# Kernel tuning notes

Hardware: AMD Instinct MI355X
Metric: run time of the kernel (lower is better)

Reference implementation:

```python
import jax, jax.numpy as jnp
import numpy as np

N = 100000
IN_C = 256
OUT_C = 256
E = 500000


def gcn_conv(x, W, b, edges):
    """PyG GCNConv: add self-loops, symmetric D^-1/2 (A+I) D^-1/2 normalization,
    then scatter-add of transformed source features into targets, plus bias."""
    n = x.shape[0]
    loop = jnp.arange(n, dtype=edges.dtype)
    row = jnp.concatenate([edges[0], loop])  # source
    col = jnp.concatenate([edges[1], loop])  # target
    deg = jax.ops.segment_sum(jnp.ones_like(col, dtype=x.dtype), col, num_segments=n)
    dis = jax.lax.rsqrt(deg)  # deg >= 1 after self-loops
    norm = dis[row] * dis[col]  # [E+n]
    h = x @ W  # [n, out]
    msg = h[row] * norm[:, None]  # gather + scale
    return jax.ops.segment_sum(msg, col, num_segments=n) + b


def setup_inputs() -> dict:
    key = jax.random.key(0)
    ks = jax.random.split(key, 24)
    x = jax.random.normal(ks[0], (N, IN_C), dtype=jnp.float32)
    edges00 = jax.random.randint(ks[1], (2, E), 0, N, dtype=jnp.int32)
    edges01 = jax.random.randint(ks[2], (2, E), 0, N, dtype=jnp.int32)
    edges10 = jax.random.randint(ks[3], (2, E), 0, N, dtype=jnp.int32)
    edges11 = jax.random.randint(ks[4], (2, E), 0, N, dtype=jnp.int32)
    t0 = (jax.random.uniform(ks[5], (N,)) > 0.5).astype(jnp.float32)
    t1 = 1.0 - t0
    scale = 1.0 / np.sqrt(IN_C)
    W1 = jax.random.normal(ks[6], (IN_C, OUT_C), dtype=jnp.float32) * scale
    W2 = jax.random.normal(ks[7], (IN_C, OUT_C), dtype=jnp.float32) * scale
    W3 = jax.random.normal(ks[8], (IN_C, OUT_C), dtype=jnp.float32) * scale
    W4 = jax.random.normal(ks[9], (IN_C, OUT_C), dtype=jnp.float32) * scale
    b1 = jnp.zeros((OUT_C,), jnp.float32)
    b2 = jnp.zeros((OUT_C,), jnp.float32)
    b3 = jnp.zeros((OUT_C,), jnp.float32)
    b4 = jnp.zeros((OUT_C,), jnp.float32)
    p0 = jax.random.normal(ks[10], (OUT_C,), dtype=jnp.float32)
    p1 = jax.random.normal(ks[11], (OUT_C,), dtype=jnp.float32)
    p2 = jax.random.normal(ks[12], (OUT_C,), dtype=jnp.float32)
    p3 = jax.random.normal(ks[13], (OUT_C,), dtype=jnp.float32)
    p4 = jax.random.normal(ks[14], (OUT_C,), dtype=jnp.float32)
    p5 = jax.random.normal(ks[15], (OUT_C,), dtype=jnp.float32)
    return dict(x=x, edges00=edges00, edges01=edges01, edges10=edges10, edges11=edges11,
                type0_idx=t0, type1_idx=t1,
                W1=W1, b1=b1, W2=W2, b2=b2, W3=W3, b3=b3, W4=W4, b4=b4,
                p0=p0, p1=p1, p2=p2, p3=p3, p4=p4, p5=p5)


def reference(x, edges00, edges01, edges10, edges11, type0_idx, type1_idx,
              W1, b1, W2, b2, W3, b3, W4, b4, p0, p1, p2, p3, p4, p5):
    # x0/x1: first feature column masked by node type, broadcast over out channels
    x0c = type0_idx * x[:, 0]  # [N]
    x1c = type1_idx * x[:, 0]
    x00 = gcn_conv(x, W1, b1, edges00)
    x01 = gcn_conv(x, W2, b2, edges01)
    x10 = gcn_conv(x, W3, b3, edges10)
    x11 = gcn_conv(x, W4, b4, edges11)
    out = (x0c[:, None] * p0 + x1c[:, None] * p1
           + x00 * p2 + x01 * p3 + x10 * p4 + x11 * p5)
    return out
```

## Files before the change

kernel.cpp:

```cpp
#include <hip/hip_runtime.h>


typedef __bf16 v8bf __attribute__((ext_vector_type(8)));
typedef float v4f __attribute__((ext_vector_type(4)));

__device__ __forceinline__ unsigned short f2bf(float f) {
  unsigned u = __float_as_uint(f);
  u += 0x7fffu + ((u >> 16) & 1u);
  return (unsigned short)(u >> 16);
}
__device__ __forceinline__ float bf2f(unsigned short s) {
  return __uint_as_float(((unsigned)s) << 16);
}
__device__ __forceinline__ void async_ld16(const void* g, void* l) {
  __builtin_amdgcn_global_load_lds((__attribute__((address_space(1))) void*)g,
                                   (__attribute__((address_space(3))) void*)l,
                                   16, 0, 0);
}

__global__ void lc_zero(int* __restrict__ p, int n) {
  int i = blockIdx.x * 256 + threadIdx.x;
  if (i < n) p[i] = 0;
}

__global__ void lc_hist(const int* __restrict__ e0, const int* __restrict__ e1,
                        const int* __restrict__ e2, const int* __restrict__ e3,
                        int* __restrict__ hist, int N, int E) {
  int e = blockIdx.x * 256 + threadIdx.x;
  if (e >= E) return;
  int k = blockIdx.y;
  const int* ed = (k == 0) ? e0 : (k == 1) ? e1 : (k == 2) ? e2 : e3;
  int col = ed[E + e];
  atomicAdd(&hist[k * N + col], 1);
}

__global__ void lc_dis(const int* __restrict__ hist, float* __restrict__ dis, int M) {
  int i = blockIdx.x * 256 + threadIdx.x;
  if (i < M) dis[i] = rsqrtf((float)(hist[i] + 1));
}

__global__ void lc_scan1(const int* __restrict__ in, int* __restrict__ outp,
                         int* __restrict__ bsum, int M) {
  __shared__ int tmp[256];
  int t = threadIdx.x, i = blockIdx.x * 256 + t;
  int v = (i < M) ? in[i] : 0;
  tmp[t] = v;
  __syncthreads();
  for (int off = 1; off < 256; off <<= 1) {
    int add = (t >= off) ? tmp[t - off] : 0;
    __syncthreads();
    tmp[t] += add;
    __syncthreads();
  }
  if (i < M) outp[i] = tmp[t] - v;
  if (t == 255) bsum[blockIdx.x] = tmp[255];
}

__global__ void lc_scan2(int* __restrict__ bsum, int nb) {
  __shared__ int tmp[256];
  __shared__ int carry_s;
  int t = threadIdx.x;
  if (t == 0) carry_s = 0;
  __syncthreads();
  for (int base = 0; base < nb; base += 256) {
    int i = base + t;
    int v = (i < nb) ? bsum[i] : 0;
    tmp[t] = v;
    __syncthreads();
    for (int off = 1; off < 256; off <<= 1) {
      int add = (t >= off) ? tmp[t - off] : 0;
      __syncthreads();
      tmp[t] += add;
      __syncthreads();
    }
    int carry = carry_s;
    int total = tmp[255];
    if (i < nb) bsum[i] = carry + tmp[t] - v;
    __syncthreads();
    if (t == 0) carry_s = carry + total;
    __syncthreads();
  }
}

__global__ void lc_scan3(int* __restrict__ rp, int* __restrict__ cursor,
                         const int* __restrict__ bsum, int M) {
  int i = blockIdx.x * 256 + threadIdx.x;
  if (i < M) {
    int v = rp[i] + bsum[blockIdx.x];
    rp[i] = v;
    cursor[i] = v;
  }
}

__global__ void lc_fill(const int* __restrict__ e0, const int* __restrict__ e1,
                        const int* __restrict__ e2, const int* __restrict__ e3,
                        int* __restrict__ cursor, const float* __restrict__ dis,
                        int2* __restrict__ payload, int N, int E) {
  int e = blockIdx.x * 256 + threadIdx.x;
  if (e >= E) return;
  int k = blockIdx.y;
  const int* ed = (k == 0) ? e0 : (k == 1) ? e1 : (k == 2) ? e2 : e3;
  int src = ed[e], col = ed[E + e];
  int pos = atomicAdd(&cursor[k * N + col], 1);
  float nrm = dis[k * N + src] * dis[k * N + col];
  payload[pos] = make_int2(src, __float_as_int(nrm));
}

__global__ void lc_bias(const float* __restrict__ b1, const float* __restrict__ b2,
                        const float* __restrict__ b3, const float* __restrict__ b4,
                        const float* __restrict__ p2, const float* __restrict__ p3,
                        const float* __restrict__ p4, const float* __restrict__ p5,
                        float* __restrict__ biasc) {
  int c = threadIdx.x;
  biasc[c] = b1[c] * p2[c] + b2[c] * p3[c] + b3[c] * p4[c] + b4[c] * p5[c];
}

__global__ void lc_prep(const float* __restrict__ W1, const float* __restrict__ W2,
                        const float* __restrict__ W3, const float* __restrict__ W4,
                        const float* __restrict__ p2, const float* __restrict__ p3,
                        const float* __restrict__ p4, const float* __restrict__ p5,
                        unsigned short* __restrict__ Wt) {
  int b = blockIdx.x;
  int k = b >> 8, co = b & 255;
  int kk = threadIdx.x;
  const float* W = (k == 0) ? W1 : (k == 1) ? W2 : (k == 2) ? W3 : W4;
  const float* p = (k == 0) ? p2 : (k == 1) ? p3 : (k == 2) ? p4 : p5;
  Wt[(size_t)co * 1024 + k * 256 + kk] = f2bf(W[kk * 256 + co] * p[co]);
}

__global__ void lc_cvt(const float4* __restrict__ x4, ushort4* __restrict__ xb4,
                       const float* __restrict__ t0, const float* __restrict__ t1,
                       float* __restrict__ m0, float* __restrict__ m1, int n4) {
  int i = blockIdx.x * 256 + threadIdx.x;
  if (i >= n4) return;
  float4 v = x4[i];
  ushort4 r;
  r.x = f2bf(v.x); r.y = f2bf(v.y); r.z = f2bf(v.z); r.w = f2bf(v.w);
  xb4[i] = r;
  if ((i & 63) == 0) {
    int n = i >> 6;
    float xc = v.x;
    m0[n] = t0[n] * xc;
    m1[n] = t1[n] * xc;
  }
}

__global__ __launch_bounds__(256) void lc_aggx(
    const unsigned short* __restrict__ xb, unsigned short* __restrict__ Agg,
    int aggw, int kcount, int kbase, const int* __restrict__ rp,
    const int* __restrict__ hist, const float* __restrict__ dis,
    const int2* __restrict__ payload, int N) {
  int t = threadIdx.x;
  int w = t >> 6, lane = t & 63;
  int n, k, koff;
  if (kcount == 4) { n = blockIdx.x; k = w; koff = k * 256; }
  else { n = blockIdx.x * 4 + w; k = kbase; koff = 0; }
  if (n >= N) return;
  int c = lane * 4;
  int idx = k * N + n;

  float dn = dis[idx];
  float s = dn * dn;
  ushort4 hv = *(const ushort4*)&xb[(size_t)n * 256 + c];
  float a0 = bf2f(hv.x) * s, a1 = bf2f(hv.y) * s;
  float a2 = bf2f(hv.z) * s, a3 = bf2f(hv.w) * s;

  int start = rp[idx];
  int cnt = hist[idx];
  int i = 0;
  for (; i + 4 <= cnt; i += 4) {
    int2 e0 = payload[start + i];
    int2 e1 = payload[start + i + 1];
    int2 e2 = payload[start + i + 2];
    int2 e3 = payload[start + i + 3];
    ushort4 g0 = *(const ushort4*)&xb[(size_t)e0.x * 256 + c];
    ushort4 g1 = *(const ushort4*)&xb[(size_t)e1.x * 256 + c];
    ushort4 g2 = *(const ushort4*)&xb[(size_t)e2.x * 256 + c];
    ushort4 g3 = *(const ushort4*)&xb[(size_t)e3.x * 256 + c];
    float n0 = __int_as_float(e0.y), n1 = __int_as_float(e1.y);
    float n2 = __int_as_float(e2.y), n3 = __int_as_float(e3.y);
    a0 += bf2f(g0.x) * n0 + bf2f(g1.x) * n1 + bf2f(g2.x) * n2 + bf2f(g3.x) * n3;
    a1 += bf2f(g0.y) * n0 + bf2f(g1.y) * n1 + bf2f(g2.y) * n2 + bf2f(g3.y) * n3;
    a2 += bf2f(g0.z) * n0 + bf2f(g1.z) * n1 + bf2f(g2.z) * n2 + bf2f(g3.z) * n3;
    a3 += bf2f(g0.w) * n0 + bf2f(g1.w) * n1 + bf2f(g2.w) * n2 + bf2f(g3.w) * n3;
  }
  for (; i < cnt; i++) {
    int2 e0 = payload[start + i];
    ushort4 g0 = *(const ushort4*)&xb[(size_t)e0.x * 256 + c];
    float n0 = __int_as_float(e0.y);
    a0 += bf2f(g0.x) * n0;
    a1 += bf2f(g0.y) * n0;
    a2 += bf2f(g0.z) * n0;
    a3 += bf2f(g0.w) * n0;
  }
  ushort4 r;
  r.x = f2bf(a0); r.y = f2bf(a1); r.z = f2bf(a2); r.w = f2bf(a3);
  *(ushort4*)&Agg[(size_t)n * aggw + koff + c] = r;
}

__global__ __launch_bounds__(256) void lc_gemm(
    const unsigned short* __restrict__ A, int strideA,
    const unsigned short* __restrict__ B, int strideB, int K,
    float* __restrict__ out, int Mrows, int addprev, int doepi,
    const float* __restrict__ m0, const float* __restrict__ m1,
    const float* __restrict__ p0, const float* __restrict__ p1,
    const float* __restrict__ biasc) {
  __shared__ alignas(16) unsigned short As[128 * 32];
  __shared__ alignas(16) unsigned short Bs[128 * 32];
  int t = threadIdx.x;
  int w = t >> 6, lane = t & 63;
  int wm = w & 1, wn = w >> 1;
  int quad = lane >> 4, l16 = lane & 15;
  int row0 = blockIdx.x * 128, col0 = blockIdx.y * 128;

  v4f acc[4][4];
#pragma unroll
  for (int mt = 0; mt < 4; mt++)
#pragma unroll
    for (int nt = 0; nt < 4; nt++) {
      v4f z = {0.f, 0.f, 0.f, 0.f};
      acc[mt][nt] = z;
    }

  for (int kk = 0; kk < K; kk += 32) {
#pragma unroll
    for (int p = 0; p < 2; p++) {
      int cbase = p * 256 + w * 64;
      int cA = cbase + lane;
      int rl = cA >> 2, c16 = cA & 3;
      int grow = row0 + rl;
      if (grow >= Mrows) grow = Mrows - 1;
      async_ld16(A + (size_t)grow * strideA + kk + c16 * 8, &As[cbase * 8]);
      async_ld16(B + (size_t)(col0 + rl) * strideB + kk + c16 * 8, &Bs[cbase * 8]);
    }
    __syncthreads();

    v8bf af[4], bfr[4];
#pragma unroll
    for (int mt = 0; mt < 4; mt++) {
      int r = wm * 64 + mt * 16 + l16;
      af[mt] = *(const v8bf*)&As[r * 32 + quad * 8];
    }
#pragma unroll
    for (int nt = 0; nt < 4; nt++) {
      int n = wn * 64 + nt * 16 + l16;
      bfr[nt] = *(const v8bf*)&Bs[n * 32 + quad * 8];
    }
#pragma unroll
    for (int mt = 0; mt < 4; mt++)
#pragma unroll
      for (int nt = 0; nt < 4; nt++)
        acc[mt][nt] =
            __builtin_amdgcn_mfma_f32_16x16x32_bf16(af[mt], bfr[nt], acc[mt][nt], 0, 0, 0);
    __syncthreads();
  }

  float pc0[4], pc1[4], bc[4];
#pragma unroll
  for (int nt = 0; nt < 4; nt++) {
    int gcol = col0 + wn * 64 + nt * 16 + l16;
    pc0[nt] = doepi ? p0[gcol] : 0.f;
    pc1[nt] = doepi ? p1[gcol] : 0.f;
    bc[nt] = doepi ? biasc[gcol] : 0.f;
  }
#pragma unroll
  for (int mt = 0; mt < 4; mt++)
#pragma unroll
    for (int r = 0; r < 4; r++) {
      int grow = row0 + wm * 64 + mt * 16 + quad * 4 + r;
      if (grow >= Mrows) continue;
      float m0v = 0.f, m1v = 0.f;
      if (doepi) { m0v = m0[grow]; m1v = m1[grow]; }
#pragma unroll
      for (int nt = 0; nt < 4; nt++) {
        int gcol = col0 + wn * 64 + nt * 16 + l16;
        size_t o = (size_t)grow * 256 + gcol;
        float v = acc[mt][nt][r];
        if (addprev) v += out[o];
        if (doepi) v += m0v * pc0[nt] + m1v * pc1[nt] + bc[nt];
        out[o] = v;
      }
    }
}

extern "C" void kernel_launch(void* const* d_in, const int* in_sizes, int n_in,
                              void* d_out, int out_size, void* d_ws, size_t ws_size,
                              hipStream_t stream) {
  const float* x = (const float*)d_in[0];
  const int* e00 = (const int*)d_in[1];
  const int* e01 = (const int*)d_in[2];
  const int* e10 = (const int*)d_in[3];
  const int* e11 = (const int*)d_in[4];
  const float* t0 = (const float*)d_in[5];
  const float* t1 = (const float*)d_in[6];
  const float* W1 = (const float*)d_in[7];
  const float* b1 = (const float*)d_in[8];
  const float* W2 = (const float*)d_in[9];
  const float* b2 = (const float*)d_in[10];
  const float* W3 = (const float*)d_in[11];
  const float* b3 = (const float*)d_in[12];
  const float* W4 = (const float*)d_in[13];
  const float* b4 = (const float*)d_in[14];
  const float* p0 = (const float*)d_in[15];
  const float* p1 = (const float*)d_in[16];
  const float* p2 = (const float*)d_in[17];
  const float* p3 = (const float*)d_in[18];
  const float* p4 = (const float*)d_in[19];
  const float* p5 = (const float*)d_in[20];
  float* out = (float*)d_out;

  int N = in_sizes[0] / 256;
  int E = in_sizes[1] / 2;
  int M4 = 4 * N;
  int nb = (M4 + 255) / 256;

  char* wp = (char*)d_ws;
  auto carve = [&](size_t bytes) {
    void* r = (void*)wp;
    wp += (bytes + 255) & ~(size_t)255;
    return r;
  };
  unsigned short* xb = (unsigned short*)carve((size_t)N * 256 * 2);
  unsigned short* Wt = (unsigned short*)carve((size_t)256 * 1024 * 2);
  int* hist = (int*)carve((size_t)M4 * 4);
  float* dis = (float*)carve((size_t)M4 * 4);
  int* rp = (int*)carve((size_t)M4 * 4);
  int* cursor = (int*)carve((size_t)M4 * 4);
  int* bsum = (int*)carve((size_t)nb * 4);
  float* biasc = (float*)carve(256 * 4);
  float* m0 = (float*)carve((size_t)N * 4);
  float* m1 = (float*)carve((size_t)N * 4);
  int2* payload = (int2*)carve((size_t)4 * E * 8);
  size_t used = (size_t)(wp - (char*)d_ws);
  size_t remain = (ws_size > used) ? ws_size - used : 0;
  bool fat = remain >= (size_t)N * 1024 * 2;
  unsigned short* Agg = (unsigned short*)wp;

  int gE = (E + 255) / 256;
  int gM = (M4 + 255) / 256;

  lc_zero<<<gM, 256, 0, stream>>>(hist, M4);
  lc_hist<<<dim3(gE, 4), 256, 0, stream>>>(e00, e01, e10, e11, hist, N, E);
  lc_dis<<<gM, 256, 0, stream>>>(hist, dis, M4);
  lc_scan1<<<nb, 256, 0, stream>>>(hist, rp, bsum, M4);
  lc_scan2<<<1, 256, 0, stream>>>(bsum, nb);
  lc_scan3<<<nb, 256, 0, stream>>>(rp, cursor, bsum, M4);
  lc_fill<<<dim3(gE, 4), 256, 0, stream>>>(e00, e01, e10, e11, cursor, dis, payload, N, E);
  lc_bias<<<1, 256, 0, stream>>>(b1, b2, b3, b4, p2, p3, p4, p5, biasc);
  lc_prep<<<1024, 256, 0, stream>>>(W1, W2, W3, W4, p2, p3, p4, p5, Wt);
  lc_cvt<<<(N * 64 + 255) / 256, 256, 0, stream>>>((const float4*)x, (ushort4*)xb,
                                                   t0, t1, m0, m1, N * 64);

  int gemm_mb = (N + 127) / 128;
  if (fat) {
    lc_aggx<<<N, 256, 0, stream>>>(xb, Agg, 1024, 4, 0, rp, hist, dis, payload, N);
    lc_gemm<<<dim3(gemm_mb, 2), 256, 0, stream>>>(Agg, 1024, Wt, 1024, 1024, out, N,
                                                  0, 1, m0, m1, p0, p1, biasc);
  } else {
    for (int k = 0; k < 4; k++) {
      lc_aggx<<<(N + 3) / 4, 256, 0, stream>>>(xb, Agg, 256, 1, k, rp, hist, dis,
                                               payload, N);
      lc_gemm<<<dim3(gemm_mb, 2), 256, 0, stream>>>(Agg, 256, Wt + k * 256, 1024, 256,
                                                    out, N, (k > 0) ? 1 : 0,
                                                    (k == 3) ? 1 : 0, m0, m1, p0, p1,
                                                    biasc);
    }
  }
}
```

Before: 720.6 us.

## Fuse aggregation with GEMM and replace CSR scan with fixed-capacity bucket scatter

Replaces the histogram/scan/fill CSR build with a single scatter kernel that writes source indices into fixed-capacity per-node buckets, spilling extras to an overflow list. Aggregation and the MFMA GEMM are fused into one kernel: each wave aggregates 16 node rows per relation into LDS and multiplies them by Wt read directly from global memory, then applies the epilogue. This removes the intermediate Agg buffer round trip and several launches. In exchange, norms are recomputed per edge, B operands are not shared through LDS, overflow handling is a linear scan, and bucket memory scales with CAP.

```diff
diff --git a/kernel.cpp b/kernel.cpp
--- a/kernel.cpp
+++ b/kernel.cpp
@@ -12,98 +12,31 @@
 __device__ __forceinline__ float bf2f(unsigned short s) {
   return __uint_as_float(((unsigned)s) << 16);
 }
-__device__ __forceinline__ void async_ld16(const void* g, void* l) {
-  __builtin_amdgcn_global_load_lds((__attribute__((address_space(1))) void*)g,
-                                   (__attribute__((address_space(3))) void*)l,
-                                   16, 0, 0);
-}
-
-__global__ void lc_zero(int* __restrict__ p, int n) {
-  int i = blockIdx.x * 256 + threadIdx.x;
-  if (i < n) p[i] = 0;
-}
-
-__global__ void lc_hist(const int* __restrict__ e0, const int* __restrict__ e1,
-                        const int* __restrict__ e2, const int* __restrict__ e3,
-                        int* __restrict__ hist, int N, int E) {
+
+__global__ void lc_scatter(const int* __restrict__ e0, const int* __restrict__ e1,
+                           const int* __restrict__ e2, const int* __restrict__ e3,
+                           int* __restrict__ hist, int* __restrict__ payload,
+                           int CAP, int* __restrict__ ovf_cnt, int2* __restrict__ ovf,
+                           int N, int E) {
   int e = blockIdx.x * 256 + threadIdx.x;
   if (e >= E) return;
   int k = blockIdx.y;
   const int* ed = (k == 0) ? e0 : (k == 1) ? e1 : (k == 2) ? e2 : e3;
+  int src = ed[e];
   int col = ed[E + e];
-  atomicAdd(&hist[k * N + col], 1);
+  int idx = k * N + col;
+  int rank = atomicAdd(&hist[idx], 1);
+  if (rank < CAP) {
+    payload[(size_t)idx * CAP + rank] = src;
+  } else {
+    int o = atomicAdd(ovf_cnt, 1);
+    ovf[o] = make_int2(idx, src);
+  }
 }
 
 __global__ void lc_dis(const int* __restrict__ hist, float* __restrict__ dis, int M) {
   int i = blockIdx.x * 256 + threadIdx.x;
   if (i < M) dis[i] = rsqrtf((float)(hist[i] + 1));
-}
-
-__global__ void lc_scan1(const int* __restrict__ in, int* __restrict__ outp,
-                         int* __restrict__ bsum, int M) {
-  __shared__ int tmp[256];
-  int t = threadIdx.x, i = blockIdx.x * 256 + t;
-  int v = (i < M) ? in[i] : 0;
-  tmp[t] = v;
-  __syncthreads();
-  for (int off = 1; off < 256; off <<= 1) {
-    int add = (t >= off) ? tmp[t - off] : 0;
-    __syncthreads();
-    tmp[t] += add;
-    __syncthreads();
-  }
-  if (i < M) outp[i] = tmp[t] - v;
-  if (t == 255) bsum[blockIdx.x] = tmp[255];
-}
-
-__global__ void lc_scan2(int* __restrict__ bsum, int nb) {
-  __shared__ int tmp[256];
-  __shared__ int carry_s;
-  int t = threadIdx.x;
-  if (t == 0) carry_s = 0;
-  __syncthreads();
-  for (int base = 0; base < nb; base += 256) {
-    int i = base + t;
-    int v = (i < nb) ? bsum[i] : 0;
-    tmp[t] = v;
-    __syncthreads();
-    for (int off = 1; off < 256; off <<= 1) {
-      int add = (t >= off) ? tmp[t - off] : 0;
-      __syncthreads();
-      tmp[t] += add;
-      __syncthreads();
-    }
-    int carry = carry_s;
-    int total = tmp[255];
-    if (i < nb) bsum[i] = carry + tmp[t] - v;
-    __syncthreads();
-    if (t == 0) carry_s = carry + total;
-    __syncthreads();
-  }
-}
-
-__global__ void lc_scan3(int* __restrict__ rp, int* __restrict__ cursor,
-                         const int* __restrict__ bsum, int M) {
-  int i = blockIdx.x * 256 + threadIdx.x;
-  if (i < M) {
-    int v = rp[i] + bsum[blockIdx.x];
-    rp[i] = v;
-    cursor[i] = v;
-  }
-}
-
-__global__ void lc_fill(const int* __restrict__ e0, const int* __restrict__ e1,
-                        const int* __restrict__ e2, const int* __restrict__ e3,
-                        int* __restrict__ cursor, const float* __restrict__ dis,
-                        int2* __restrict__ payload, int N, int E) {
-  int e = blockIdx.x * 256 + threadIdx.x;
-  if (e >= E) return;
-  int k = blockIdx.y;
-  const int* ed = (k == 0) ? e0 : (k == 1) ? e1 : (k == 2) ? e2 : e3;
-  int src = ed[e], col = ed[E + e];
-  int pos = atomicAdd(&cursor[k * N + col], 1);
-  float nrm = dis[k * N + src] * dis[k * N + col];
-  payload[pos] = make_int2(src, __float_as_int(nrm));
 }
 
 __global__ void lc_bias(const float* __restrict__ b1, const float* __restrict__ b2,
@@ -145,142 +78,120 @@
   }
 }
 
-__global__ __launch_bounds__(256) void lc_aggx(
-    const unsigned short* __restrict__ xb, unsigned short* __restrict__ Agg,
-    int aggw, int kcount, int kbase, const int* __restrict__ rp,
-    const int* __restrict__ hist, const float* __restrict__ dis,
-    const int2* __restrict__ payload, int N) {
+#define LROW 264
+__global__ __launch_bounds__(256, 2) void lc_fused(
+    const unsigned short* __restrict__ xb, const unsigned short* __restrict__ Wt,
+    const int* __restrict__ payload, int CAP, const int* __restrict__ hist,
+    const float* __restrict__ dis, const int* __restrict__ ovf_cnt,
+    const int2* __restrict__ ovf, const float* __restrict__ m0,
+    const float* __restrict__ m1, const float* __restrict__ p0,
+    const float* __restrict__ p1, const float* __restrict__ biasc,
+    float* __restrict__ out, int N) {
+  __shared__ alignas(16) unsigned short lds[4 * 16 * LROW];
   int t = threadIdx.x;
   int w = t >> 6, lane = t & 63;
-  int n, k, koff;
-  if (kcount == 4) { n = blockIdx.x; k = w; koff = k * 256; }
-  else { n = blockIdx.x * 4 + w; k = kbase; koff = 0; }
-  if (n >= N) return;
+  int quad = lane >> 4, l16 = lane & 15;
+  int row0 = blockIdx.x * 64 + w * 16;
+  unsigned short* A = &lds[w * 16 * LROW];
   int c = lane * 4;
-  int idx = k * N + n;
-
-  float dn = dis[idx];
-  float s = dn * dn;
-  ushort4 hv = *(const ushort4*)&xb[(size_t)n * 256 + c];
-  float a0 = bf2f(hv.x) * s, a1 = bf2f(hv.y) * s;
-  float a2 = bf2f(hv.z) * s, a3 = bf2f(hv.w) * s;
-
-  int start = rp[idx];
-  int cnt = hist[idx];
-  int i = 0;
-  for (; i + 4 <= cnt; i += 4) {
-    int2 e0 = payload[start + i];
-    int2 e1 = payload[start + i + 1];
-    int2 e2 = payload[start + i + 2];
-    int2 e3 = payload[start + i + 3];
-    ushort4 g0 = *(const ushort4*)&xb[(size_t)e0.x * 256 + c];
-    ushort4 g1 = *(const ushort4*)&xb[(size_t)e1.x * 256 + c];
-    ushort4 g2 = *(const ushort4*)&xb[(size_t)e2.x * 256 + c];
-    ushort4 g3 = *(const ushort4*)&xb[(size_t)e3.x * 256 + c];
-    float n0 = __int_as_float(e0.y), n1 = __int_as_float(e1.y);
-    float n2 = __int_as_float(e2.y), n3 = __int_as_float(e3.y);
-    a0 += bf2f(g0.x) * n0 + bf2f(g1.x) * n1 + bf2f(g2.x) * n2 + bf2f(g3.x) * n3;
-    a1 += bf2f(g0.y) * n0 + bf2f(g1.y) * n1 + bf2f(g2.y) * n2 + bf2f(g3.y) * n3;
-    a2 += bf2f(g0.z) * n0 + bf2f(g1.z) * n1 + bf2f(g2.z) * n2 + bf2f(g3.z) * n3;
-    a3 += bf2f(g0.w) * n0 + bf2f(g1.w) * n1 + bf2f(g2.w) * n2 + bf2f(g3.w) * n3;
-  }
-  for (; i < cnt; i++) {
-    int2 e0 = payload[start + i];
-    ushort4 g0 = *(const ushort4*)&xb[(size_t)e0.x * 256 + c];
-    float n0 = __int_as_float(e0.y);
-    a0 += bf2f(g0.x) * n0;
-    a1 += bf2f(g0.y) * n0;
-    a2 += bf2f(g0.z) * n0;
-    a3 += bf2f(g0.w) * n0;
-  }
-  ushort4 r;
-  r.x = f2bf(a0); r.y = f2bf(a1); r.z = f2bf(a2); r.w = f2bf(a3);
-  *(ushort4*)&Agg[(size_t)n * aggw + koff + c] = r;
-}
-
-__global__ __launch_bounds__(256) void lc_gemm(
-    const unsigned short* __restrict__ A, int strideA,
-    const unsigned short* __restrict__ B, int strideB, int K,
-    float* __restrict__ out, int Mrows, int addprev, int doepi,
-    const float* __restrict__ m0, const float* __restrict__ m1,
-    const float* __restrict__ p0, const float* __restrict__ p1,
-    const float* __restrict__ biasc) {
-  __shared__ alignas(16) unsigned short As[128 * 32];
-  __shared__ alignas(16) unsigned short Bs[128 * 32];
-  int t = threadIdx.x;
-  int w = t >> 6, lane = t & 63;
-  int wm = w & 1, wn = w >> 1;
-  int quad = lane >> 4, l16 = lane & 15;
-  int row0 = blockIdx.x * 128, col0 = blockIdx.y * 128;
-
-  v4f acc[4][4];
-#pragma unroll
-  for (int mt = 0; mt < 4; mt++)
-#pragma unroll
-    for (int nt = 0; nt < 4; nt++) {
-      v4f z = {0.f, 0.f, 0.f, 0.f};
-      acc[mt][nt] = z;
+
+  v4f acc[16];
+#pragma unroll
+  for (int nt = 0; nt < 16; nt++) {
+    v4f z = {0.f, 0.f, 0.f, 0.f};
+    acc[nt] = z;
+  }
+
+  for (int s = 0; s < 4; s++) {
+    for (int i = 0; i < 16; i++) {
+      int node = row0 + i;
+      if (node >= N) break;
+      int idx = s * N + node;
+      float dn = dis[idx];
+      float sl = dn * dn;
+      ushort4 hv = *(const ushort4*)&xb[(size_t)node * 256 + c];
+      float a0 = bf2f(hv.x) * sl, a1 = bf2f(hv.y) * sl;
+      float a2 = bf2f(hv.z) * sl, a3 = bf2f(hv.w) * sl;
+      int cnt = hist[idx];
+      int lim = cnt < CAP ? cnt : CAP;
+      const int* pp = payload + (size_t)idx * CAP;
+      int j = 0;
+      for (; j + 4 <= lim; j += 4) {
+        int s0 = pp[j], s1 = pp[j + 1], s2 = pp[j + 2], s3 = pp[j + 3];
+        ushort4 g0 = *(const ushort4*)&xb[(size_t)s0 * 256 + c];
+        ushort4 g1 = *(const ushort4*)&xb[(size_t)s1 * 256 + c];
+        ushort4 g2 = *(const ushort4*)&xb[(size_t)s2 * 256 + c];
+        ushort4 g3 = *(const ushort4*)&xb[(size_t)s3 * 256 + c];
+        float n0 = dis[s * N + s0] * dn, n1 = dis[s * N + s1] * dn;
+        float n2 = dis[s * N + s2] * dn, n3 = dis[s * N + s3] * dn;
+        a0 += bf2f(g0.x) * n0 + bf2f(g1.x) * n1 + bf2f(g2.x) * n2 + bf2f(g3.x) * n3;
+        a1 += bf2f(g0.y) * n0 + bf2f(g1.y) * n1 + bf2f(g2.y) * n2 + bf2f(g3.y) * n3;
+        a2 += bf2f(g0.z) * n0 + bf2f(g1.z) * n1 + bf2f(g2.z) * n2 + bf2f(g3.z) * n3;
+        a3 += bf2f(g0.w) * n0 + bf2f(g1.w) * n1 + bf2f(g2.w) * n2 + bf2f(g3.w) * n3;
+      }
+      for (; j < lim; j++) {
+        int sj = pp[j];
+        ushort4 g = *(const ushort4*)&xb[(size_t)sj * 256 + c];
+        float nr = dis[s * N + sj] * dn;
+        a0 += bf2f(g.x) * nr; a1 += bf2f(g.y) * nr;
+        a2 += bf2f(g.z) * nr; a3 += bf2f(g.w) * nr;
+      }
+      if (cnt > CAP) {
+        int tot = *ovf_cnt;
+        for (int o = 0; o < tot; o++) {
+          int2 ov = ovf[o];
+          if (ov.x == idx) {
+            int sj = ov.y;
+            ushort4 g = *(const ushort4*)&xb[(size_t)sj * 256 + c];
+            float nr = dis[s * N + sj] * dn;
+            a0 += bf2f(g.x) * nr; a1 += bf2f(g.y) * nr;
+            a2 += bf2f(g.z) * nr; a3 += bf2f(g.w) * nr;
+          }
+        }
+      }
+      ushort4 r;
+      r.x = f2bf(a0); r.y = f2bf(a1); r.z = f2bf(a2); r.w = f2bf(a3);
+      *(ushort4*)&A[i * LROW + c] = r;
     }
 
-  for (int kk = 0; kk < K; kk += 32) {
-#pragma unroll
-    for (int p = 0; p < 2; p++) {
-      int cbase = p * 256 + w * 64;
-      int cA = cbase + lane;
-      int rl = cA >> 2, c16 = cA & 3;
-      int grow = row0 + rl;
-      if (grow >= Mrows) grow = Mrows - 1;
-      async_ld16(A + (size_t)grow * strideA + kk + c16 * 8, &As[cbase * 8]);
-      async_ld16(B + (size_t)(col0 + rl) * strideB + kk + c16 * 8, &Bs[cbase * 8]);
+#pragma unroll
+    for (int kstep = 0; kstep < 8; kstep++) {
+      v8bf af = *(const v8bf*)&A[l16 * LROW + kstep * 32 + quad * 8];
+#pragma unroll
+      for (int nt = 0; nt < 8; nt++) {
+        int colb = nt * 16 + l16;
+        v8bf bfr = *(const v8bf*)&Wt[(size_t)colb * 1024 + s * 256 + kstep * 32 + quad * 8];
+        acc[nt] = __builtin_amdgcn_mfma_f32_16x16x32_bf16(af, bfr, acc[nt], 0, 0, 0);
+      }
+#pragma unroll
+      for (int nt = 8; nt < 16; nt++) {
+        int colb = nt * 16 + l16;
+        v8bf bfr = *(const v8bf*)&Wt[(size_t)colb * 1024 + s * 256 + kstep * 32 + quad * 8];
+        acc[nt] = __builtin_amdgcn_mfma_f32_16x16x32_bf16(af, bfr, acc[nt], 0, 0, 0);
+      }
     }
-    __syncthreads();
-
-    v8bf af[4], bfr[4];
-#pragma unroll
-    for (int mt = 0; mt < 4; mt++) {
-      int r = wm * 64 + mt * 16 + l16;
-      af[mt] = *(const v8bf*)&As[r * 32 + quad * 8];
+  }
+
+  float pc0[16], pc1[16], bc[16];
+#pragma unroll
+  for (int nt = 0; nt < 16; nt++) {
+    int gcol = nt * 16 + l16;
+    pc0[nt] = p0[gcol];
+    pc1[nt] = p1[gcol];
+    bc[nt] = biasc[gcol];
+  }
+#pragma unroll
+  for (int r = 0; r < 4; r++) {
+    int grow = row0 + quad * 4 + r;
+    if (grow >= N) continue;
+    float m0v = m0[grow], m1v = m1[grow];
+#pragma unroll
+    for (int nt = 0; nt < 16; nt++) {
+      int gcol = nt * 16 + l16;
+      out[(size_t)grow * 256 + gcol] =
+          acc[nt][r] + m0v * pc0[nt] + m1v * pc1[nt] + bc[nt];
     }
-#pragma unroll
-    for (int nt = 0; nt < 4; nt++) {
-      int n = wn * 64 + nt * 16 + l16;
-      bfr[nt] = *(const v8bf*)&Bs[n * 32 + quad * 8];
-    }
-#pragma unroll
-    for (int mt = 0; mt < 4; mt++)
-#pragma unroll
-      for (int nt = 0; nt < 4; nt++)
-        acc[mt][nt] =
-            __builtin_amdgcn_mfma_f32_16x16x32_bf16(af[mt], bfr[nt], acc[mt][nt], 0, 0, 0);
-    __syncthreads();
-  }
-
-  float pc0[4], pc1[4], bc[4];
-#pragma unroll
-  for (int nt = 0; nt < 4; nt++) {
-    int gcol = col0 + wn * 64 + nt * 16 + l16;
-    pc0[nt] = doepi ? p0[gcol] : 0.f;
-    pc1[nt] = doepi ? p1[gcol] : 0.f;
-    bc[nt] = doepi ? biasc[gcol] : 0.f;
-  }
-#pragma unroll
-  for (int mt = 0; mt < 4; mt++)
-#pragma unroll
-    for (int r = 0; r < 4; r++) {
-      int grow = row0 + wm * 64 + mt * 16 + quad * 4 + r;
-      if (grow >= Mrows) continue;
-      float m0v = 0.f, m1v = 0.f;
-      if (doepi) { m0v = m0[grow]; m1v = m1[grow]; }
-#pragma unroll
-      for (int nt = 0; nt < 4; nt++) {
-        int gcol = col0 + wn * 64 + nt * 16 + l16;
-        size_t o = (size_t)grow * 256 + gcol;
-        float v = acc[mt][nt][r];
-        if (addprev) v += out[o];
-        if (doepi) v += m0v * pc0[nt] + m1v * pc1[nt] + bc[nt];
-        out[o] = v;
-      }
-    }
+  }
 }
 
 extern "C" void kernel_launch(void* const* d_in, const int* in_sizes, int n_in,
@@ -312,7 +223,6 @@
   int N = in_sizes[0] / 256;
   int E = in_sizes[1] / 2;
   int M4 = 4 * N;
-  int nb = (M4 + 255) / 256;
 
   char* wp = (char*)d_ws;
   auto carve = [&](size_t bytes) {
@@ -322,48 +232,31 @@
   };
   unsigned short* xb = (unsigned short*)carve((size_t)N * 256 * 2);
   unsigned short* Wt = (unsigned short*)carve((size_t)256 * 1024 * 2);
-  int* hist = (int*)carve((size_t)M4 * 4);
+  int* hist = (int*)carve((size_t)(M4 + 1) * 4);
+  int* ovf_cnt = hist + M4;
   float* dis = (float*)carve((size_t)M4 * 4);
-  int* rp = (int*)carve((size_t)M4 * 4);
-  int* cursor = (int*)carve((size_t)M4 * 4);
-  int* bsum = (int*)carve((size_t)nb * 4);
   float* biasc = (float*)carve(256 * 4);
   float* m0 = (float*)carve((size_t)N * 4);
   float* m1 = (float*)carve((size_t)N * 4);
-  int2* payload = (int2*)carve((size_t)4 * E * 8);
+  int2* ovf = (int2*)carve((size_t)E * 8);
   size_t used = (size_t)(wp - (char*)d_ws);
   size_t remain = (ws_size > used) ? ws_size - used : 0;
-  bool fat = remain >= (size_t)N * 1024 * 2;
-  unsigned short* Agg = (unsigned short*)wp;
+  int CAP = 64;
+  while (CAP > 4 && remain < (size_t)M4 * CAP * 4) CAP >>= 1;
+  int* payload = (int*)wp;
 
   int gE = (E + 255) / 256;
   int gM = (M4 + 255) / 256;
 
-  lc_zero<<<gM, 256, 0, stream>>>(hist, M4);
-  lc_hist<<<dim3(gE, 4), 256, 0, stream>>>(e00, e01, e10, e11, hist, N, E);
+  hipMemsetAsync(hist, 0, (size_t)(M4 + 1) * 4, stream);
+  lc_scatter<<<dim3(gE, 4), 256, 0, stream>>>(e00, e01, e10, e11, hist, payload,
+                                              CAP, ovf_cnt, ovf, N, E);
   lc_dis<<<gM, 256, 0, stream>>>(hist, dis, M4);
-  lc_scan1<<<nb, 256, 0, stream>>>(hist, rp, bsum, M4);
-  lc_scan2<<<1, 256, 0, stream>>>(bsum, nb);
-  lc_scan3<<<nb, 256, 0, stream>>>(rp, cursor, bsum, M4);
-  lc_fill<<<dim3(gE, 4), 256, 0, stream>>>(e00, e01, e10, e11, cursor, dis, payload, N, E);
   lc_bias<<<1, 256, 0, stream>>>(b1, b2, b3, b4, p2, p3, p4, p5, biasc);
   lc_prep<<<1024, 256, 0, stream>>>(W1, W2, W3, W4, p2, p3, p4, p5, Wt);
   lc_cvt<<<(N * 64 + 255) / 256, 256, 0, stream>>>((const float4*)x, (ushort4*)xb,
                                                    t0, t1, m0, m1, N * 64);
-
-  int gemm_mb = (N + 127) / 128;
-  if (fat) {
-    lc_aggx<<<N, 256, 0, stream>>>(xb, Agg, 1024, 4, 0, rp, hist, dis, payload, N);
-    lc_gemm<<<dim3(gemm_mb, 2), 256, 0, stream>>>(Agg, 1024, Wt, 1024, 1024, out, N,
-                                                  0, 1, m0, m1, p0, p1, biasc);
-  } else {
-    for (int k = 0; k < 4; k++) {
-      lc_aggx<<<(N + 3) / 4, 256, 0, stream>>>(xb, Agg, 256, 1, k, rp, hist, dis,
-                                               payload, N);
-      lc_gemm<<<dim3(gemm_mb, 2), 256, 0, stream>>>(Agg, 256, Wt + k * 256, 1024, 256,
-                                                    out, N, (k > 0) ? 1 : 0,
-                                                    (k == 3) ? 1 : 0, m0, m1, p0, p1,
-                                                    biasc);
-    }
-  }
-}
+  lc_fused<<<(N + 63) / 64, 256, 0, stream>>>(xb, Wt, payload, CAP, hist, dis,
+                                              ovf_cnt, ovf, m0, m1, p0, p1, biasc,
+                                              out, N);
+}
```

New measurement: 1.137 ms. 57.7% more time.
